# Optimization experiments

Measured on AMD Instinct MI355X. Metric: run time of the kernel, lower is better.

## Reference

```python
import jax, jax.numpy as jnp
import numpy as np

N = 100000
IN_C = 128
HID = 128
LAT = 64
E = 800000


def gcn_conv(x, src, dst, norm, W, b, num_nodes):
    # x: [N, Cin]; src/dst: [E+N] (self-loops appended); norm: [E+N]
    xw = x @ W                                   # [N, Cout]
    msg = xw[src] * norm[:, None]                # gather + scale, [E+N, Cout]
    out = jax.ops.segment_sum(msg, dst, num_segments=num_nodes)
    return out + b


def setup_inputs() -> dict:
    key = jax.random.key(0)
    ks = jax.random.split(key, 8)
    x = jax.random.normal(ks[0], (N, IN_C), dtype=jnp.float32)
    edge_index = jax.random.randint(ks[1], (2, E), 0, N, dtype=jnp.int64)
    batch = jnp.zeros((N,), dtype=jnp.int64)
    # GCNConv params (Glorot-ish scale)
    W1 = jax.random.normal(ks[2], (IN_C, HID), dtype=jnp.float32) / np.sqrt(IN_C)
    b1 = jnp.zeros((HID,), dtype=jnp.float32)
    Wmu = jax.random.normal(ks[3], (HID, LAT), dtype=jnp.float32) / np.sqrt(HID)
    bmu = jnp.zeros((LAT,), dtype=jnp.float32)
    Wlv = jax.random.normal(ks[4], (HID, LAT), dtype=jnp.float32) / np.sqrt(HID)
    blv = jnp.zeros((LAT,), dtype=jnp.float32)
    return {"x": x, "edge_index": edge_index, "batch": batch,
            "W1": W1, "b1": b1, "Wmu": Wmu, "bmu": bmu, "Wlv": Wlv, "blv": blv}


def reference(x, edge_index, batch, W1, b1, Wmu, bmu, Wlv, blv):
    num_nodes = x.shape[0]
    loop = jnp.arange(num_nodes, dtype=edge_index.dtype)
    src = jnp.concatenate([edge_index[0], loop])   # source nodes (+self loops)
    dst = jnp.concatenate([edge_index[1], loop])   # target nodes (+self loops)
    # symmetric GCN normalization: deg over targets, norm = d[src]^-1/2 * d[dst]^-1/2
    deg = jax.ops.segment_sum(jnp.ones_like(dst, dtype=x.dtype), dst,
                              num_segments=num_nodes)
    dis = jnp.where(deg > 0, jax.lax.rsqrt(deg), 0.0)
    norm = dis[src] * dis[dst]                      # [E+N]

    h = jax.nn.relu(gcn_conv(x, src, dst, norm, W1, b1, num_nodes))
    mu = gcn_conv(h, src, dst, norm, Wmu, bmu, num_nodes)
    logvar = gcn_conv(h, src, dst, norm, Wlv, blv, num_nodes)
    return (mu, logvar)
```

## Files before the change

kernel.cpp:

```cpp
#include <hip/hip_runtime.h>

typedef short bf16x8 __attribute__((ext_vector_type(8)));
typedef float f32x4 __attribute__((ext_vector_type(4)));

#define ELLK 32
#define OCAP 4096
#define CSTRIDE 16

static __device__ __forceinline__ float4 f4zero() { return make_float4(0.f, 0.f, 0.f, 0.f); }

static __device__ __forceinline__ unsigned short f2bf(float f) {
  unsigned u = __float_as_uint(f);
  u += 0x7FFFu + ((u >> 16) & 1u);
  return (unsigned short)(u >> 16);
}
static __device__ __forceinline__ float2 bf2x2(unsigned u) {
  float2 r;
  r.x = __uint_as_float(u << 16);
  r.y = __uint_as_float(u & 0xFFFF0000u);
  return r;
}

__global__ void k_setup(const float* __restrict__ W1, const float* __restrict__ Wmu,
                        const float* __restrict__ Wlv, unsigned short* __restrict__ Wt1,
                        unsigned short* __restrict__ Wt2, uint4* __restrict__ cntz,
                        int* __restrict__ ocount, unsigned* __restrict__ A,
                        unsigned* __restrict__ H, int nz4, int nbz, int n) {
  int b = blockIdx.x;
  if (b < nbz) {
    int i = b * 256 + threadIdx.x;
    if (i < nz4) cntz[i] = make_uint4(0u, 0u, 0u, 0u);
    if (b == 0) {
      int t = threadIdx.x;
      if (t == 0) *ocount = 0;
      if (t < 64) A[(size_t)n * 64 + t] = 0u;
      else if (t < 128) H[(size_t)n * 64 + (t - 64)] = 0u;
    }
  } else {
    int id = (b - nbz) * 256 + threadIdx.x;
    if (id < 16384) {
      int j = id & 7, lane = (id >> 3) & 63, g = id >> 9;
      int kk = g >> 3, nt = g & 7, li = lane & 15, quad = lane >> 4;
      int nn = nt * 16 + li, k = kk * 32 + quad * 8 + j;
      Wt1[id] = f2bf(W1[k * 128 + nn]);
    } else {
      int id2 = id - 16384;
      int j = id2 & 7, lane = (id2 >> 3) & 63, g = id2 >> 9;
      int kk = g >> 3, nt = g & 7, li = lane & 15, quad = lane >> 4;
      int nn = nt * 16 + li, k = kk * 32 + quad * 8 + j;
      float v = (nn < 64) ? Wmu[k * 64 + nn] : Wlv[k * 64 + (nn - 64)];
      Wt2[id2] = f2bf(v);
    }
  }
}

__global__ void k_fill(const int* __restrict__ ei, int* __restrict__ cnt,
                       int* __restrict__ ell, int2* __restrict__ ovf,
                       int* __restrict__ ocount, int E, int n) {
  int e0 = blockIdx.x * 1024 + threadIdx.x;
  int ss[4], dd[4], pos[4];
  bool ok[4];
#pragma unroll
  for (int k = 0; k < 4; ++k) {
    int e = e0 + k * 256;
    ok[k] = (e < E);
    ss[k] = ok[k] ? ei[e] : 0;
    dd[k] = ok[k] ? ei[E + e] : 0;
  }
#pragma unroll
  for (int k = 0; k < 4; ++k)
    pos[k] = ok[k] ? atomicAdd(&cnt[(size_t)dd[k] * CSTRIDE], 1) : ELLK;
#pragma unroll
  for (int k = 0; k < 4; ++k) {
    if (!ok[k]) continue;
    if (pos[k] < ELLK) {
      ell[(size_t)pos[k] * n + dd[k]] = ss[k];
    } else {
      int o = atomicAdd(ocount, 1);
      if (o < OCAP) ovf[o] = make_int2(dd[k], ss[k]);
    }
  }
}

__global__ __launch_bounds__(256, 6) void k_gemm1(
    const float* __restrict__ x, const unsigned short* __restrict__ Wt,
    const int* __restrict__ cnt, unsigned short* __restrict__ A,
    float* __restrict__ dnorm, unsigned* __restrict__ mflag, int n) {
  __shared__ unsigned short Xl[64 * 136];
  __shared__ float dnl[64];
  const int tid = threadIdx.x;
  const int row0 = blockIdx.x * 64;
  {
#pragma unroll
    for (int i = 0; i < 8; ++i) {
      int idx = tid + i * 256;
      int r = idx >> 5, c = idx & 31;
      int gi = row0 + r;
      float4 v = (gi < n) ? ((const float4*)x)[(size_t)gi * 32 + c] : f4zero();
      ushort4 p;
      p.x = f2bf(v.x); p.y = f2bf(v.y); p.z = f2bf(v.z); p.w = f2bf(v.w);
      *(ushort4*)&Xl[r * 136 + c * 4] = p;
    }
  }
  if (tid < 64) {
    int gi = row0 + tid;
    float dn = 0.f;
    if (gi < n) {
      int c = cnt[(size_t)gi * CSTRIDE];
      dn = rsqrtf((float)(c + 1));
      dnorm[gi] = dn;
      int mm = (c < ELLK) ? c : ELLK;
      mflag[gi] = (unsigned)mm | ((c > ELLK) ? 0x80000000u : 0u);
    }
    dnl[tid] = dn;
  }
  __syncthreads();

  const int wave = tid >> 6, lane = tid & 63;
  const int li = lane & 15, quad = lane >> 4;
  const int m0 = wave * 16;
  const bf16x8* Wf = (const bf16x8*)Wt;
  f32x4 acc[8];
#pragma unroll
  for (int t = 0; t < 8; ++t) acc[t] = (f32x4){0.f, 0.f, 0.f, 0.f};
#pragma unroll
  for (int kk = 0; kk < 4; ++kk) {
    int ko = kk * 32 + quad * 8;
    bf16x8 a = *(const bf16x8*)&Xl[(m0 + li) * 136 + ko];
    bf16x8 bf[8];
#pragma unroll
    for (int nt = 0; nt < 8; ++nt) bf[nt] = Wf[(kk * 8 + nt) * 64 + lane];
#pragma unroll
    for (int nt = 0; nt < 8; ++nt)
      acc[nt] = __builtin_amdgcn_mfma_f32_16x16x32_bf16(a, bf[nt], acc[nt], 0, 0, 0);
  }
  __syncthreads();
  float dn[4];
#pragma unroll
  for (int r = 0; r < 4; ++r) dn[r] = dnl[m0 + quad * 4 + r];
#pragma unroll
  for (int nt = 0; nt < 8; ++nt)
#pragma unroll
    for (int r = 0; r < 4; ++r)
      Xl[(m0 + quad * 4 + r) * 136 + nt * 16 + li] = f2bf(acc[nt][r] * dn[r]);
  __syncthreads();
  {
    uint4* A4 = (uint4*)A;
#pragma unroll
    for (int i = 0; i < 4; ++i) {
      int idx = tid + i * 256;
      int r = idx >> 4, c = idx & 15;
      int gi = row0 + r;
      if (gi < n) A4[(size_t)gi * 16 + c] = *(uint4*)&Xl[r * 136 + c * 8];
    }
  }
}

__global__ __launch_bounds__(256, 8) void k_spmm1(
    const unsigned* __restrict__ mflag, const float* __restrict__ dnorm,
    const int* __restrict__ ell, const int2* __restrict__ ovf,
    const int* __restrict__ ocount, const unsigned* __restrict__ S,
    unsigned* __restrict__ D, const float2* __restrict__ bias, int n) {
  int wid = (blockIdx.x * blockDim.x + threadIdx.x) >> 6;
  if (wid >= n) return;
  int lane = threadIdx.x & 63;
  unsigned mf = mflag[wid];
  int m = (int)(mf & 0xFFFFu);
  float dsd = dnorm[wid];
  float2 acc = bf2x2(S[(size_t)wid * 64 + lane]);
  const int* ep = ell + wid;
  int nbt = (m + 7) >> 3;
  for (int b = 0; b < nbt; ++b) {
    int j0 = b * 8;
    int idx[8];
#pragma unroll
    for (int k = 0; k < 8; ++k) idx[k] = ep[(size_t)(j0 + k) * n];
#pragma unroll
    for (int k = 0; k < 8; ++k) idx[k] = (j0 + k < m) ? idx[k] : n;
    unsigned u[8];
#pragma unroll
    for (int k = 0; k < 8; ++k) u[k] = S[(size_t)idx[k] * 64 + lane];
#pragma unroll
    for (int k = 0; k < 8; ++k) {
      float2 f = bf2x2(u[k]);
      acc.x += f.x;
      acc.y += f.y;
    }
  }
  if (mf & 0x80000000u) {
    int oc = *ocount;
    if (oc > OCAP) oc = OCAP;
    for (int k = 0; k < oc; ++k) {
      int2 e = ovf[k];
      if (e.x == wid) {
        float2 u0 = bf2x2(S[(size_t)e.y * 64 + lane]);
        acc.x += u0.x;
        acc.y += u0.y;
      }
    }
  }
  float2 b = bias[lane];
  float2 o;
  o.x = dsd * fmaxf(fmaf(dsd, acc.x, b.x), 0.f);
  o.y = dsd * fmaxf(fmaf(dsd, acc.y, b.y), 0.f);
  unsigned pk = (unsigned)f2bf(o.x) | ((unsigned)f2bf(o.y) << 16);
  D[(size_t)wid * 64 + lane] = pk;
}

__global__ __launch_bounds__(256, 8) void k_spmm2_gemm2(
    const unsigned* __restrict__ mflag, const float* __restrict__ dnorm,
    const int* __restrict__ ell, const int2* __restrict__ ovf,
    const int* __restrict__ ocount, const unsigned* __restrict__ H,
    const unsigned short* __restrict__ Wt, const float* __restrict__ bmu,
    const float* __restrict__ blv, float* __restrict__ out, int n) {
  __shared__ unsigned short Xl[64 * 136];
  const int tid = threadIdx.x;
  const int wave = tid >> 6, lane = tid & 63;
  const int row0 = blockIdx.x * 64;
#pragma unroll 1
  for (int i = 0; i < 16; ++i) {
    int nd = row0 + wave * 16 + i;
    unsigned pk = 0u;
    if (nd < n) {
      unsigned mf = mflag[nd];
      int m = (int)(mf & 0xFFFFu);
      float dsd = dnorm[nd];
      float2 acc = bf2x2(H[(size_t)nd * 64 + lane]);
      const int* ep = ell + nd;
      int nbt = (m + 7) >> 3;
      for (int b = 0; b < nbt; ++b) {
        int j0 = b * 8;
        int idx[8];
#pragma unroll
        for (int k = 0; k < 8; ++k) idx[k] = ep[(size_t)(j0 + k) * n];
#pragma unroll
        for (int k = 0; k < 8; ++k) idx[k] = (j0 + k < m) ? idx[k] : n;
        unsigned u[8];
#pragma unroll
        for (int k = 0; k < 8; ++k) u[k] = H[(size_t)idx[k] * 64 + lane];
#pragma unroll
        for (int k = 0; k < 8; ++k) {
          float2 f = bf2x2(u[k]);
          acc.x += f.x;
          acc.y += f.y;
        }
      }
      if (mf & 0x80000000u) {
        int oc = *ocount;
        if (oc > OCAP) oc = OCAP;
        for (int k = 0; k < oc; ++k) {
          int2 e = ovf[k];
          if (e.x == nd) {
            float2 u0 = bf2x2(H[(size_t)e.y * 64 + lane]);
            acc.x += u0.x;
            acc.y += u0.y;
          }
        }
      }
      float2 o;
      o.x = dsd * acc.x;
      o.y = dsd * acc.y;
      pk = (unsigned)f2bf(o.x) | ((unsigned)f2bf(o.y) << 16);
    }
    *(unsigned*)&Xl[(wave * 16 + i) * 136 + 2 * lane] = pk;
  }
  __syncthreads();

  const int li = lane & 15, quad = lane >> 4;
  const int m0 = wave * 16;
  const bf16x8* Wf = (const bf16x8*)Wt;
  float bias[8];
#pragma unroll
  for (int nt = 0; nt < 8; ++nt) {
    int c = nt * 16 + li;
    bias[nt] = (c < 64) ? bmu[c] : blv[c - 64];
  }
  f32x4 acc[8];
#pragma unroll
  for (int t = 0; t < 8; ++t) acc[t] = (f32x4){0.f, 0.f, 0.f, 0.f};
#pragma unroll
  for (int kk = 0; kk < 4; ++kk) {
    int ko = kk * 32 + quad * 8;
    bf16x8 a = *(const bf16x8*)&Xl[(m0 + li) * 136 + ko];
    bf16x8 bf[8];
#pragma unroll
    for (int nt = 0; nt < 8; ++nt) bf[nt] = Wf[(kk * 8 + nt) * 64 + lane];
#pragma unroll
    for (int nt = 0; nt < 8; ++nt)
      acc[nt] = __builtin_amdgcn_mfma_f32_16x16x32_bf16(a, bf[nt], acc[nt], 0, 0, 0);
  }
#pragma unroll
  for (int nt = 0; nt < 8; ++nt) {
    int col = nt * 16 + li;
#pragma unroll
    for (int r = 0; r < 4; ++r) {
      int gi = row0 + m0 + quad * 4 + r;
      if (gi < n) {
        float v = acc[nt][r] + bias[nt];
        if (col < 64) out[(size_t)gi * 64 + col] = v;
        else          out[(size_t)(n + gi) * 64 + (col - 64)] = v;
      }
    }
  }
}

extern "C" void kernel_launch(void* const* d_in, const int* in_sizes, int n_in,
                              void* d_out, int out_size, void* d_ws, size_t ws_size,
                              hipStream_t stream) {
  const float* x   = (const float*)d_in[0];
  const int*   ei  = (const int*)d_in[1];
  const float* W1  = (const float*)d_in[3];
  const float* b1  = (const float*)d_in[4];
  const float* Wmu = (const float*)d_in[5];
  const float* bmu = (const float*)d_in[6];
  const float* Wlv = (const float*)d_in[7];
  const float* blv = (const float*)d_in[8];
  float* out = (float*)d_out;

  const int n = in_sizes[0] / 128;
  const int E = in_sizes[1] / 2;

  float* ws = (float*)d_ws;
  size_t p = 0;
  int* cnt    = (int*)(ws + p); p += (size_t)n * CSTRIDE;
  int* ocount = (int*)(ws + p); p += 1;
  p = (p + 3) & ~(size_t)3;
  int* ell    = (int*)(ws + p); p += (size_t)n * ELLK;
  int2* ovf   = (int2*)(ws + p); p += (size_t)OCAP * 2;
  unsigned* A = (unsigned*)(ws + p); p += (size_t)(n + 1) * 64;
  unsigned* H = (unsigned*)(ws + p); p += (size_t)(n + 1) * 64;
  unsigned short* Wt1 = (unsigned short*)(ws + p); p += 8192;
  unsigned short* Wt2 = (unsigned short*)(ws + p); p += 8192;
  float* dnorm    = (float*)(ws + p); p += n;
  unsigned* mflag = (unsigned*)(ws + p); p += n;

  int nz4  = (n * CSTRIDE) / 4;
  int nbz  = (nz4 + 255) / 256;
  int eb   = (E + 1023) / 1024;
  int gblk = (n + 63) / 64;
  int sblk = (n + 3) / 4;

  k_setup<<<nbz + 128, 256, 0, stream>>>(W1, Wmu, Wlv, Wt1, Wt2, (uint4*)cnt, ocount,
                                         A, H, nz4, nbz, n);
  k_fill<<<eb, 256, 0, stream>>>(ei, cnt, ell, ovf, ocount, E, n);
  k_gemm1<<<gblk, 256, 0, stream>>>(x, Wt1, cnt, (unsigned short*)A, dnorm, mflag, n);
  k_spmm1<<<sblk, 256, 0, stream>>>(mflag, dnorm, ell, ovf, ocount, A, H,
                                    (const float2*)b1, n);
  k_spmm2_gemm2<<<gblk, 256, 0, stream>>>(mflag, dnorm, ell, ovf, ocount, H, Wt2,
                                          bmu, blv, out, n);
}
```

Measured before the change: 274.2 us.

## Load GEMM1 A fragments directly from global and balance SpMM rows via LDS work queue

In k_gemm1 the x tile is no longer staged through shared memory. Each lane loads its own float4 pair straight from global memory, converts it to bf16 and feeds the MFMA, which removes one LDS round trip and one barrier. In k_spmm2_gemm2 the fixed split of 16 rows per wave is replaced by a shared atomic counter that hands out rows dynamically, balancing the uneven per-row degree across waves. The costs are less coalesced global loads for x and one LDS atomic plus a shuffle per row.

Result: no change. 271.6 us (-0.9%).

```diff
diff --git a/kernel.cpp b/kernel.cpp
--- a/kernel.cpp
+++ b/kernel.cpp
@@ -90,18 +90,6 @@
   __shared__ float dnl[64];
   const int tid = threadIdx.x;
   const int row0 = blockIdx.x * 64;
-  {
-#pragma unroll
-    for (int i = 0; i < 8; ++i) {
-      int idx = tid + i * 256;
-      int r = idx >> 5, c = idx & 31;
-      int gi = row0 + r;
-      float4 v = (gi < n) ? ((const float4*)x)[(size_t)gi * 32 + c] : f4zero();
-      ushort4 p;
-      p.x = f2bf(v.x); p.y = f2bf(v.y); p.z = f2bf(v.z); p.w = f2bf(v.w);
-      *(ushort4*)&Xl[r * 136 + c * 4] = p;
-    }
-  }
   if (tid < 64) {
     int gi = row0 + tid;
     float dn = 0.f;
@@ -120,13 +108,21 @@
   const int li = lane & 15, quad = lane >> 4;
   const int m0 = wave * 16;
   const bf16x8* Wf = (const bf16x8*)Wt;
+
+  const int arow = row0 + m0 + li;
+  const bool rok = (arow < n);
+  const float4* xr = (const float4*)x + (size_t)(rok ? arow : 0) * 32;
+
   f32x4 acc[8];
 #pragma unroll
   for (int t = 0; t < 8; ++t) acc[t] = (f32x4){0.f, 0.f, 0.f, 0.f};
 #pragma unroll
   for (int kk = 0; kk < 4; ++kk) {
-    int ko = kk * 32 + quad * 8;
-    bf16x8 a = *(const bf16x8*)&Xl[(m0 + li) * 136 + ko];
+    float4 v0 = rok ? xr[kk * 8 + quad * 2] : f4zero();
+    float4 v1 = rok ? xr[kk * 8 + quad * 2 + 1] : f4zero();
+    bf16x8 a = (bf16x8){(short)f2bf(v0.x), (short)f2bf(v0.y), (short)f2bf(v0.z),
+                        (short)f2bf(v0.w), (short)f2bf(v1.x), (short)f2bf(v1.y),
+                        (short)f2bf(v1.z), (short)f2bf(v1.w)};
     bf16x8 bf[8];
 #pragma unroll
     for (int nt = 0; nt < 8; ++nt) bf[nt] = Wf[(kk * 8 + nt) * 64 + lane];
@@ -134,7 +130,6 @@
     for (int nt = 0; nt < 8; ++nt)
       acc[nt] = __builtin_amdgcn_mfma_f32_16x16x32_bf16(a, bf[nt], acc[nt], 0, 0, 0);
   }
-  __syncthreads();
   float dn[4];
 #pragma unroll
   for (int r = 0; r < 4; ++r) dn[r] = dnl[m0 + quad * 4 + r];
@@ -214,12 +209,19 @@
     const unsigned short* __restrict__ Wt, const float* __restrict__ bmu,
     const float* __restrict__ blv, float* __restrict__ out, int n) {
   __shared__ unsigned short Xl[64 * 136];
+  __shared__ int wq;
   const int tid = threadIdx.x;
   const int wave = tid >> 6, lane = tid & 63;
   const int row0 = blockIdx.x * 64;
-#pragma unroll 1
-  for (int i = 0; i < 16; ++i) {
-    int nd = row0 + wave * 16 + i;
+  if (tid == 0) wq = 0;
+  __syncthreads();
+
+  for (;;) {
+    int iloc = 0;
+    if (lane == 0) iloc = atomicAdd(&wq, 1);
+    iloc = __shfl(iloc, 0);
+    if (iloc >= 64) break;
+    int nd = row0 + iloc;
     unsigned pk = 0u;
     if (nd < n) {
       unsigned mf = mflag[nd];
@@ -262,7 +264,7 @@
       o.y = dsd * acc.y;
       pk = (unsigned)f2bf(o.x) | ((unsigned)f2bf(o.y) << 16);
     }
-    *(unsigned*)&Xl[(wave * 16 + i) * 136 + 2 * lane] = pk;
+    *(unsigned*)&Xl[iloc * 136 + 2 * lane] = pk;
   }
   __syncthreads();
 
```
